# Optimization experiments

Measured on AMD Instinct MI355X. Metric: run time of the kernel, lower is better.

## Reference

```python
import jax, jax.numpy as jnp
import numpy as np

B, S, D, F, E, NS, K = 2, 1024, 1024, 4096, 8, 8, 2
FS = F // NS  # shared-expert hidden size = d_ff // num_shared_experts


def setup_inputs() -> dict:
    key = jax.random.key(0)
    ks = jax.random.split(key, 8)
    scale = 0.02
    return {
        "hidden_states": jax.random.normal(ks[0], (B, S, D), jnp.float32),
        "gate_W": jax.random.normal(ks[1], (E, D), jnp.float32) * scale,
        "w1_e": jax.random.normal(ks[2], (E, D, F), jnp.float32) * scale,
        "w3_e": jax.random.normal(ks[3], (E, D, F), jnp.float32) * scale,
        "w2_e": jax.random.normal(ks[4], (E, F, D), jnp.float32) * scale,
        "w1_s": jax.random.normal(ks[5], (NS, D, FS), jnp.float32) * scale,
        "w3_s": jax.random.normal(ks[6], (NS, D, FS), jnp.float32) * scale,
        "w2_s": jax.random.normal(ks[7], (NS, FS, D), jnp.float32) * scale,
    }


def reference(hidden_states, gate_W, w1_e, w3_e, w2_e, w1_s, w3_s, w2_s):
    b, s, d = hidden_states.shape
    e = gate_W.shape[0]
    flat = hidden_states.reshape(-1, d)            # [T, D]
    T = flat.shape[0]

    # --- gate: softmax over experts, top-k probs scattered (k=0 slot only survives) ---
    logits = (flat @ gate_W.T).astype(jnp.float32)  # [T, E]
    probs = jax.nn.softmax(logits, axis=-1)
    top_v, top_i = jax.lax.top_k(probs, K)          # [T, K]
    gates = jnp.zeros((T, e), probs.dtype).at[jnp.arange(T)[:, None], top_i].set(top_v)

    # --- routed experts: module runs every expert densely on all tokens ---
    g = jax.nn.silu(jnp.einsum('td,edf->etf', flat, w1_e))  # [E, T, F]
    u = jnp.einsum('td,edf->etf', flat, w3_e)
    out_e = jnp.einsum('etf,efd->etd', g * u, w2_e)         # [E, T, D]
    routed = jnp.einsum('te,etd->td', gates, out_e).reshape(b, s, d)

    # --- shared experts (mean over NS experts) ---
    gs = jax.nn.silu(jnp.einsum('bsd,ndf->nbsf', hidden_states, w1_s))
    us = jnp.einsum('bsd,ndf->nbsf', hidden_states, w3_s)
    shared = jnp.einsum('nbsf,nfd->bsd', gs * us, w2_s) / w1_s.shape[0]

    alpha = 0.5
    return alpha * shared + (1.0 - alpha) * routed
```

## Files before the change

kernel.cpp:

```cpp
#include <hip/hip_runtime.h>

#define T 2048
#define D 1024
#define F 4096
#define E 8
#define NS 8
#define FS 512
#define SHB 5120
#define NROWS 7168
#define MT_MAX 56

typedef float floatx4 __attribute__((ext_vector_type(4)));
typedef short short8 __attribute__((ext_vector_type(8)));

__device__ __forceinline__ unsigned short f2bf(float f) {
  unsigned int u = __float_as_uint(f);
  u += 0x7FFF + ((u >> 16) & 1);
  return (unsigned short)(u >> 16);
}

__device__ __forceinline__ void glds16(const void* g, void* l) {
  __builtin_amdgcn_global_load_lds(
      (const __attribute__((address_space(1))) void*)g,
      (__attribute__((address_space(3))) void*)l, 16, 0, 0);
}

__global__ void gate_kernel(const float* __restrict__ x, const float* __restrict__ gW,
                            unsigned short* __restrict__ xb, int* __restrict__ cnt,
                            int* __restrict__ list_tok, float* __restrict__ list_gate) {
  int t = blockIdx.x, tid = threadIdx.x;
  const float* xr = x + (size_t)t * D;
  float acc[E];
#pragma unroll
  for (int e = 0; e < E; ++e) acc[e] = 0.f;
  for (int d = tid; d < D; d += 256) {
    float xv = xr[d];
    xb[(size_t)t * D + d] = f2bf(xv);
#pragma unroll
    for (int e = 0; e < E; ++e) acc[e] += xv * gW[e * D + d];
  }
#pragma unroll
  for (int o = 32; o > 0; o >>= 1)
#pragma unroll
    for (int e = 0; e < E; ++e) acc[e] += __shfl_down(acc[e], o, 64);
  __shared__ float wred[4][E];
  int lane = tid & 63, wv = tid >> 6;
  if (lane == 0)
#pragma unroll
    for (int e = 0; e < E; ++e) wred[wv][e] = acc[e];
  __syncthreads();
  if (tid == 0) {
    float l[E];
#pragma unroll
    for (int e = 0; e < E; ++e) l[e] = wred[0][e] + wred[1][e] + wred[2][e] + wred[3][e];
    int i1 = 0; float m1 = l[0];
    for (int e = 1; e < E; ++e) if (l[e] > m1) { m1 = l[e]; i1 = e; }
    int i2 = -1; float m2 = -3.4e38f;
    for (int e = 0; e < E; ++e) if (e != i1 && l[e] > m2) { m2 = l[e]; i2 = e; }
    float s = 0.f, p[E];
#pragma unroll
    for (int e = 0; e < E; ++e) { p[e] = __expf(l[e] - m1); s += p[e]; }
    float inv = 1.f / s;
    int p1 = atomicAdd(&cnt[i1], 1);
    list_tok[i1 * T + p1] = t; list_gate[i1 * T + p1] = p[i1] * inv;
    int p2 = atomicAdd(&cnt[i2], 1);
    list_tok[i2 * T + p2] = t; list_gate[i2 * T + p2] = p[i2] * inv;
  }
}

__global__ void offsets_kernel(const int* __restrict__ cnt, int* __restrict__ off,
                               int* __restrict__ mt_expert) {
  if (threadIdx.x == 0 && blockIdx.x == 0) {
    int o = 0;
    for (int e = 0; e < E; ++e) { off[e] = o; o += (cnt[e] + 127) & ~127; }
    off[E] = o;
    for (int i = 0; i < MT_MAX; ++i) mt_expert[i] = -1;
    for (int e = 0; e < E; ++e) {
      int t0 = off[e] >> 7, nt = (cnt[e] + 127) >> 7;
      for (int i = 0; i < nt; ++i) mt_expert[t0 + i] = e;
    }
    for (int i = SHB >> 7; i < MT_MAX; ++i) mt_expert[i] = E;
  }
}

__global__ void scatter_kernel(const int* __restrict__ cnt, const int* __restrict__ off,
                               const int* __restrict__ list_tok, const float* __restrict__ list_gate,
                               int* __restrict__ tok_of_row, float* __restrict__ row_scale,
                               int* __restrict__ tok_rows, int* __restrict__ tk) {
  int idx = blockIdx.x * 256 + threadIdx.x;
  int e = idx >> 11, i = idx & (T - 1);
  if (e < E && i < cnt[e]) {
    int row = off[e] + i;
    int t = list_tok[e * T + i];
    tok_of_row[row] = t;
    row_scale[row] = 0.5f * list_gate[e * T + i];
    int k = atomicAdd(&tk[t], 1);
    tok_rows[2 * t + k] = row;
  }
}

__global__ void transpose_cast(const float* __restrict__ in, unsigned short* __restrict__ out,
                               int R, int C) {
  in += (size_t)blockIdx.z * R * C;
  out += (size_t)blockIdx.z * R * C;
  int r0 = blockIdx.y * 32, c0 = blockIdx.x * 32;
  __shared__ float tile[32][33];
  int tid = threadIdx.x;
#pragma unroll
  for (int p = 0; p < 4; ++p) {
    int idx = p * 256 + tid;
    int rl = idx >> 5, cl = idx & 31;
    tile[rl][cl] = in[(size_t)(r0 + rl) * C + c0 + cl];
  }
  __syncthreads();
  int Rt = R >> 5;
#pragma unroll
  for (int p = 0; p < 4; ++p) {
    int idx = p * 256 + tid;
    int cl = idx >> 5, rl = idx & 31;
    int c = c0 + cl, r = r0 + rl;
    size_t o = ((size_t)(c >> 7) * Rt + (r >> 5)) * 4096 + (size_t)(c & 127) * 32 + (r & 31);
    out[o] = f2bf(tile[rl][cl]);
  }
}

__global__ __launch_bounds__(256, 2) void up_gemm(
    const unsigned short* __restrict__ xb, const unsigned short* __restrict__ W1T,
    const unsigned short* __restrict__ W3T, const unsigned short* __restrict__ W1sT,
    const unsigned short* __restrict__ W3sT, const int* __restrict__ cnt,
    const int* __restrict__ off, const int* __restrict__ tok_of_row,
    unsigned short* __restrict__ Hb) {
  int e = blockIdx.z, mtile = blockIdx.y, ntile = blockIdx.x;
  int hbase;
  const unsigned short *B1, *B3;
  if (e < E) {
    int Me = cnt[e];
    if (mtile * 128 >= Me) return;
    hbase = off[e];
    B1 = W1T + (size_t)e * F * D;
    B3 = W3T + (size_t)e * F * D;
  } else {
    hbase = SHB;
    B1 = W1sT; B3 = W3sT;
  }
  __shared__ unsigned short Al[128 * 32];
  __shared__ unsigned short B1l[128 * 32];
  __shared__ unsigned short B3l[128 * 32];
  int tid = threadIdx.x;
  int lane = tid & 63, wv = tid >> 6, wm = wv >> 1, wn = wv & 1;
  int row16 = lane & 15, quad = lane >> 4;

  int ar = tid >> 1;
  int lrow = mtile * 128 + ar;
  int srow = (e < E) ? tok_of_row[hbase + lrow] : lrow;
  const uint4* aptr = (const uint4*)(xb + (size_t)srow * D) + (tid & 1) * 2;
  uint4* alds = (uint4*)Al + ar * 4 + (tid & 1) * 2;

  const unsigned short* b1t = B1 + (size_t)ntile * (D / 32) * 4096;
  const unsigned short* b3t = B3 + (size_t)ntile * (D / 32) * 4096;

  floatx4 accg[4][4], accu[4][4];
#pragma unroll
  for (int i = 0; i < 4; ++i)
#pragma unroll
    for (int j = 0; j < 4; ++j) {
      accg[i][j] = (floatx4){0.f, 0.f, 0.f, 0.f};
      accu[i][j] = (floatx4){0.f, 0.f, 0.f, 0.f};
    }
  int lw = wv * 1024;
  for (int kt = 0; kt < D / 32; ++kt) {
    uint4 av0 = aptr[0];
    uint4 av1 = aptr[1];
    const char* b1s = (const char*)(b1t + (size_t)kt * 4096);
    const char* b3s = (const char*)(b3t + (size_t)kt * 4096);
    glds16(b1s + tid * 16, (char*)B1l + lw);
    glds16(b1s + 4096 + tid * 16, (char*)B1l + 4096 + lw);
    glds16(b3s + tid * 16, (char*)B3l + lw);
    glds16(b3s + 4096 + tid * 16, (char*)B3l + 4096 + lw);
    alds[0] = av0; alds[1] = av1;
    __syncthreads();
    short8 af[4], b1f[4], b3f[4];
#pragma unroll
    for (int mi = 0; mi < 4; ++mi)
      af[mi] = *(const short8*)(Al + (wm * 64 + mi * 16 + row16) * 32 + quad * 8);
#pragma unroll
    for (int ni = 0; ni < 4; ++ni) {
      b1f[ni] = *(const short8*)(B1l + (wn * 64 + ni * 16 + row16) * 32 + quad * 8);
      b3f[ni] = *(const short8*)(B3l + (wn * 64 + ni * 16 + row16) * 32 + quad * 8);
    }
#pragma unroll
    for (int mi = 0; mi < 4; ++mi)
#pragma unroll
      for (int ni = 0; ni < 4; ++ni) {
        accg[mi][ni] = __builtin_amdgcn_mfma_f32_16x16x32_bf16(af[mi], b1f[ni], accg[mi][ni], 0, 0, 0);
        accu[mi][ni] = __builtin_amdgcn_mfma_f32_16x16x32_bf16(af[mi], b3f[ni], accu[mi][ni], 0, 0, 0);
      }
    aptr += 4;
    __syncthreads();
  }
#pragma unroll
  for (int mi = 0; mi < 4; ++mi)
#pragma unroll
    for (int ni = 0; ni < 4; ++ni)
#pragma unroll
      for (int r = 0; r < 4; ++r) {
        int lr = mtile * 128 + wm * 64 + mi * 16 + quad * 4 + r;
        int hrow = hbase + lr;
        int col = ntile * 128 + wn * 64 + ni * 16 + row16;
        float g = accg[mi][ni][r], u = accu[mi][ni][r];
        float h = g * u / (1.0f + __expf(-g));
        size_t o = ((size_t)(hrow >> 7) * 128 + (col >> 5)) * 4096 + (size_t)(hrow & 127) * 32 + (col & 31);
        Hb[o] = f2bf(h);
      }
}

__global__ __launch_bounds__(256, 2) void down_gemm(
    const unsigned short* __restrict__ Hb, const unsigned short* __restrict__ W2T,
    const unsigned short* __restrict__ W2sT, const int* __restrict__ mt_expert,
    const float* __restrict__ row_scale, float* __restrict__ O) {
  int mt = blockIdx.y, ntile = blockIdx.x;
  int e = mt_expert[mt];
  if (e < 0) return;
  const unsigned short* Bt = ((e < E) ? (W2T + (size_t)e * D * F) : W2sT)
                             + (size_t)ntile * (F / 32) * 4096;
  const unsigned short* At = Hb + (size_t)mt * (F / 32) * 4096;
  __shared__ unsigned short Al[128 * 32];
  __shared__ unsigned short Bl[128 * 32];
  int tid = threadIdx.x;
  int lane = tid & 63, wv = tid >> 6, wm = wv >> 1, wn = wv & 1;
  int row16 = lane & 15, quad = lane >> 4;
  floatx4 acc[4][4];
#pragma unroll
  for (int i = 0; i < 4; ++i)
#pragma unroll
    for (int j = 0; j < 4; ++j) acc[i][j] = (floatx4){0.f, 0.f, 0.f, 0.f};
  int lw = wv * 1024;
  for (int kt = 0; kt < F / 32; ++kt) {
    const char* as = (const char*)(At + (size_t)kt * 4096);
    const char* bs = (const char*)(Bt + (size_t)kt * 4096);
    glds16(as + tid * 16, (char*)Al + lw);
    glds16(as + 4096 + tid * 16, (char*)Al + 4096 + lw);
    glds16(bs + tid * 16, (char*)Bl + lw);
    glds16(bs + 4096 + tid * 16, (char*)Bl + 4096 + lw);
    __syncthreads();
    short8 af[4], bf[4];
#pragma unroll
    for (int mi = 0; mi < 4; ++mi)
      af[mi] = *(const short8*)(Al + (wm * 64 + mi * 16 + row16) * 32 + quad * 8);
#pragma unroll
    for (int ni = 0; ni < 4; ++ni)
      bf[ni] = *(const short8*)(Bl + (wn * 64 + ni * 16 + row16) * 32 + quad * 8);
#pragma unroll
    for (int mi = 0; mi < 4; ++mi)
#pragma unroll
      for (int ni = 0; ni < 4; ++ni)
        acc[mi][ni] = __builtin_amdgcn_mfma_f32_16x16x32_bf16(af[mi], bf[ni], acc[mi][ni], 0, 0, 0);
    __syncthreads();
  }
#pragma unroll
  for (int mi = 0; mi < 4; ++mi)
#pragma unroll
    for (int ni = 0; ni < 4; ++ni)
#pragma unroll
      for (int r = 0; r < 4; ++r) {
        int grow = mt * 128 + wm * 64 + mi * 16 + quad * 4 + r;
        int col = ntile * 128 + wn * 64 + ni * 16 + row16;
        float scale = (grow < SHB) ? row_scale[grow] : 0.0625f;
        O[(size_t)grow * D + col] = acc[mi][ni][r] * scale;
      }
}

__global__ void combine_kernel(const float* __restrict__ O, const int* __restrict__ tok_rows,
                               float* __restrict__ out) {
  int idx = blockIdx.x * 256 + threadIdx.x;
  int t = idx >> 8, c = idx & 255;
  int r0 = tok_rows[2 * t], r1 = tok_rows[2 * t + 1];
  const float4* O4 = (const float4*)O;
  float4 a = O4[(size_t)r0 * 256 + c];
  float4 b = O4[(size_t)r1 * 256 + c];
  float4 s = O4[((size_t)SHB + t) * 256 + c];
  float4 r;
  r.x = a.x + b.x + s.x;
  r.y = a.y + b.y + s.y;
  r.z = a.z + b.z + s.z;
  r.w = a.w + b.w + s.w;
  ((float4*)out)[idx] = r;
}

extern "C" void kernel_launch(void* const* d_in, const int* in_sizes, int n_in,
                              void* d_out, int out_size, void* d_ws, size_t ws_size,
                              hipStream_t stream) {
  (void)in_sizes; (void)n_in; (void)out_size; (void)ws_size;
  const float* x   = (const float*)d_in[0];
  const float* gW  = (const float*)d_in[1];
  const float* w1e = (const float*)d_in[2];
  const float* w3e = (const float*)d_in[3];
  const float* w2e = (const float*)d_in[4];
  const float* w1s = (const float*)d_in[5];
  const float* w3s = (const float*)d_in[6];
  const float* w2s = (const float*)d_in[7];
  float* out = (float*)d_out;

  char* w = (char*)d_ws;
  auto alloc = [&](size_t bytes) {
    char* p = w; w += (bytes + 255) & ~(size_t)255; return p;
  };
  unsigned short* xb   = (unsigned short*)alloc((size_t)T * D * 2);
  unsigned short* W1T  = (unsigned short*)alloc((size_t)E * F * D * 2);
  unsigned short* W3T  = (unsigned short*)alloc((size_t)E * F * D * 2);
  unsigned short* W2T  = (unsigned short*)alloc((size_t)E * D * F * 2);
  unsigned short* W1sT = (unsigned short*)alloc((size_t)F * D * 2);
  unsigned short* W3sT = (unsigned short*)alloc((size_t)F * D * 2);
  unsigned short* W2sT = (unsigned short*)alloc((size_t)D * F * 2);
  unsigned short* Hb   = (unsigned short*)alloc((size_t)NROWS * F * 2);
  float* Ob        = (float*)alloc((size_t)NROWS * D * 4);
  float* row_scale = (float*)alloc((size_t)SHB * 4);
  float* list_gate = (float*)alloc((size_t)E * T * 4);
  int* list_tok    = (int*)alloc((size_t)E * T * 4);
  int* tok_rows    = (int*)alloc((size_t)T * 2 * 4);
  int* offv        = (int*)alloc(16 * 4);
  int* mt_expert   = (int*)alloc(64 * 4);
  int* ctrl        = (int*)alloc((size_t)(8 + T + SHB) * 4);
  int* cnt = ctrl; int* tk = ctrl + 8; int* tok_of_row = ctrl + 8 + T;

  hipMemsetAsync(ctrl, 0, (size_t)(8 + T + SHB) * 4, stream);
  gate_kernel<<<T, 256, 0, stream>>>(x, gW, xb, cnt, list_tok, list_gate);
  offsets_kernel<<<1, 64, 0, stream>>>(cnt, offv, mt_expert);
  scatter_kernel<<<(E * T) / 256, 256, 0, stream>>>(cnt, offv, list_tok, list_gate,
                                                    tok_of_row, row_scale, tok_rows, tk);
  transpose_cast<<<dim3(F / 32, D / 32, E), 256, 0, stream>>>(w1e, W1T, D, F);
  transpose_cast<<<dim3(F / 32, D / 32, E), 256, 0, stream>>>(w3e, W3T, D, F);
  transpose_cast<<<dim3(D / 32, F / 32, E), 256, 0, stream>>>(w2e, W2T, F, D);
  transpose_cast<<<dim3(FS / 32, D / 32, NS), 256, 0, stream>>>(w1s, W1sT, D, FS);
  transpose_cast<<<dim3(FS / 32, D / 32, NS), 256, 0, stream>>>(w3s, W3sT, D, FS);
  transpose_cast<<<dim3(D / 32, F / 32, 1), 256, 0, stream>>>(w2s, W2sT, F, D);
  up_gemm<<<dim3(F / 128, 16, E + 1), 256, 0, stream>>>(xb, W1T, W3T, W1sT, W3sT,
                                                        cnt, offv, tok_of_row, Hb);
  down_gemm<<<dim3(D / 128, MT_MAX), 256, 0, stream>>>(Hb, W2T, W2sT, mt_expert, row_scale, Ob);
  combine_kernel<<<(T * D / 4) / 256, 256, 0, stream>>>(Ob, tok_rows, out);
}
```

Baseline: 777.3 us.

## Swizzle LDS tiles, split-K down GEMM, compact up grid, vectorize transpose

The transpose-cast kernel now uses float4 loads and ushort4 stores. Both GEMMs XOR-swizzle their LDS layout to avoid bank conflicts on the fragment reads. The up GEMM launches only live m-tiles through the mt_expert map. The down GEMM is split along K into two halves that write separate output buffers, which the combine kernel sums. Split-K doubles the down GEMM's parallelism but costs an extra fp32 output buffer plus more traffic in combine.

Measured after the change: 745.2 us. 1.04x faster.

```diff
diff --git a/kernel.cpp b/kernel.cpp
--- a/kernel.cpp
+++ b/kernel.cpp
@@ -106,41 +106,38 @@
   int r0 = blockIdx.y * 32, c0 = blockIdx.x * 32;
   __shared__ float tile[32][33];
   int tid = threadIdx.x;
-#pragma unroll
-  for (int p = 0; p < 4; ++p) {
-    int idx = p * 256 + tid;
-    int rl = idx >> 5, cl = idx & 31;
-    tile[rl][cl] = in[(size_t)(r0 + rl) * C + c0 + cl];
+  {
+    int rl = tid >> 3, cl = (tid & 7) * 4;
+    float4 v = *(const float4*)(in + (size_t)(r0 + rl) * C + c0 + cl);
+    tile[rl][cl] = v.x; tile[rl][cl + 1] = v.y;
+    tile[rl][cl + 2] = v.z; tile[rl][cl + 3] = v.w;
   }
   __syncthreads();
-  int Rt = R >> 5;
-#pragma unroll
-  for (int p = 0; p < 4; ++p) {
-    int idx = p * 256 + tid;
-    int cl = idx >> 5, rl = idx & 31;
-    int c = c0 + cl, r = r0 + rl;
+  {
+    int cl = tid >> 3, rq = (tid & 7) * 4;
+    int c = c0 + cl, r = r0 + rq;
+    ushort4 v;
+    v.x = f2bf(tile[rq][cl]);     v.y = f2bf(tile[rq + 1][cl]);
+    v.z = f2bf(tile[rq + 2][cl]); v.w = f2bf(tile[rq + 3][cl]);
+    int Rt = R >> 5;
     size_t o = ((size_t)(c >> 7) * Rt + (r >> 5)) * 4096 + (size_t)(c & 127) * 32 + (r & 31);
-    out[o] = f2bf(tile[rl][cl]);
+    *(ushort4*)(out + o) = v;
   }
 }
 
 __global__ __launch_bounds__(256, 2) void up_gemm(
     const unsigned short* __restrict__ xb, const unsigned short* __restrict__ W1T,
     const unsigned short* __restrict__ W3T, const unsigned short* __restrict__ W1sT,
-    const unsigned short* __restrict__ W3sT, const int* __restrict__ cnt,
-    const int* __restrict__ off, const int* __restrict__ tok_of_row,
-    unsigned short* __restrict__ Hb) {
-  int e = blockIdx.z, mtile = blockIdx.y, ntile = blockIdx.x;
-  int hbase;
+    const unsigned short* __restrict__ W3sT, const int* __restrict__ mt_expert,
+    const int* __restrict__ tok_of_row, unsigned short* __restrict__ Hb) {
+  int mt = blockIdx.y, ntile = blockIdx.x;
+  int e = mt_expert[mt];
+  if (e < 0) return;
   const unsigned short *B1, *B3;
   if (e < E) {
-    int Me = cnt[e];
-    if (mtile * 128 >= Me) return;
-    hbase = off[e];
     B1 = W1T + (size_t)e * F * D;
     B3 = W3T + (size_t)e * F * D;
   } else {
-    hbase = SHB;
     B1 = W1sT; B3 = W3sT;
   }
   __shared__ unsigned short Al[128 * 32];
@@ -149,12 +146,17 @@
   int tid = threadIdx.x;
   int lane = tid & 63, wv = tid >> 6, wm = wv >> 1, wn = wv & 1;
   int row16 = lane & 15, quad = lane >> 4;
+  int qsw8 = ((lane >> 4) ^ ((lane >> 1) & 3)) * 8;
+  int swzb = (tid & ~3) * 16 + (((tid & 3) ^ ((tid >> 3) & 3)) * 16);
 
   int ar = tid >> 1;
-  int lrow = mtile * 128 + ar;
-  int srow = (e < E) ? tok_of_row[hbase + lrow] : lrow;
-  const uint4* aptr = (const uint4*)(xb + (size_t)srow * D) + (tid & 1) * 2;
-  uint4* alds = (uint4*)Al + ar * 4 + (tid & 1) * 2;
+  int hrow_s = mt * 128 + ar;
+  int srow = (e < E) ? tok_of_row[hrow_s] : (hrow_s - SHB);
+  int ja = (tid & 1) * 2;
+  int sa = (tid >> 2) & 3;
+  const uint4* aptr = (const uint4*)(xb + (size_t)srow * D) + ja;
+  uint4* alds0 = (uint4*)Al + ar * 4 + (ja ^ sa);
+  uint4* alds1 = (uint4*)Al + ar * 4 + ((ja + 1) ^ sa);
 
   const unsigned short* b1t = B1 + (size_t)ntile * (D / 32) * 4096;
   const unsigned short* b3t = B3 + (size_t)ntile * (D / 32) * 4096;
@@ -173,20 +175,20 @@
     uint4 av1 = aptr[1];
     const char* b1s = (const char*)(b1t + (size_t)kt * 4096);
     const char* b3s = (const char*)(b3t + (size_t)kt * 4096);
-    glds16(b1s + tid * 16, (char*)B1l + lw);
-    glds16(b1s + 4096 + tid * 16, (char*)B1l + 4096 + lw);
-    glds16(b3s + tid * 16, (char*)B3l + lw);
-    glds16(b3s + 4096 + tid * 16, (char*)B3l + 4096 + lw);
-    alds[0] = av0; alds[1] = av1;
+    glds16(b1s + swzb, (char*)B1l + lw);
+    glds16(b1s + 4096 + swzb, (char*)B1l + 4096 + lw);
+    glds16(b3s + swzb, (char*)B3l + lw);
+    glds16(b3s + 4096 + swzb, (char*)B3l + 4096 + lw);
+    alds0[0] = av0; alds1[0] = av1;
     __syncthreads();
     short8 af[4], b1f[4], b3f[4];
 #pragma unroll
     for (int mi = 0; mi < 4; ++mi)
-      af[mi] = *(const short8*)(Al + (wm * 64 + mi * 16 + row16) * 32 + quad * 8);
+      af[mi] = *(const short8*)(Al + (wm * 64 + mi * 16 + row16) * 32 + qsw8);
 #pragma unroll
     for (int ni = 0; ni < 4; ++ni) {
-      b1f[ni] = *(const short8*)(B1l + (wn * 64 + ni * 16 + row16) * 32 + quad * 8);
-      b3f[ni] = *(const short8*)(B3l + (wn * 64 + ni * 16 + row16) * 32 + quad * 8);
+      b1f[ni] = *(const short8*)(B1l + (wn * 64 + ni * 16 + row16) * 32 + qsw8);
+      b3f[ni] = *(const short8*)(B3l + (wn * 64 + ni * 16 + row16) * 32 + qsw8);
     }
 #pragma unroll
     for (int mi = 0; mi < 4; ++mi)
@@ -204,8 +206,7 @@
     for (int ni = 0; ni < 4; ++ni)
 #pragma unroll
       for (int r = 0; r < 4; ++r) {
-        int lr = mtile * 128 + wm * 64 + mi * 16 + quad * 4 + r;
-        int hrow = hbase + lr;
+        int hrow = mt * 128 + wm * 64 + mi * 16 + quad * 4 + r;
         int col = ntile * 128 + wn * 64 + ni * 16 + row16;
         float g = accg[mi][ni][r], u = accu[mi][ni][r];
         float h = g * u / (1.0f + __expf(-g));
@@ -218,38 +219,41 @@
     const unsigned short* __restrict__ Hb, const unsigned short* __restrict__ W2T,
     const unsigned short* __restrict__ W2sT, const int* __restrict__ mt_expert,
     const float* __restrict__ row_scale, float* __restrict__ O) {
-  int mt = blockIdx.y, ntile = blockIdx.x;
+  int mt = blockIdx.y, ntile = blockIdx.x, kz = blockIdx.z;
   int e = mt_expert[mt];
   if (e < 0) return;
   const unsigned short* Bt = ((e < E) ? (W2T + (size_t)e * D * F) : W2sT)
                              + (size_t)ntile * (F / 32) * 4096;
   const unsigned short* At = Hb + (size_t)mt * (F / 32) * 4096;
+  O += (size_t)kz * NROWS * D;
   __shared__ unsigned short Al[128 * 32];
   __shared__ unsigned short Bl[128 * 32];
   int tid = threadIdx.x;
   int lane = tid & 63, wv = tid >> 6, wm = wv >> 1, wn = wv & 1;
   int row16 = lane & 15, quad = lane >> 4;
+  int qsw8 = ((lane >> 4) ^ ((lane >> 1) & 3)) * 8;
+  int swzb = (tid & ~3) * 16 + (((tid & 3) ^ ((tid >> 3) & 3)) * 16);
   floatx4 acc[4][4];
 #pragma unroll
   for (int i = 0; i < 4; ++i)
 #pragma unroll
     for (int j = 0; j < 4; ++j) acc[i][j] = (floatx4){0.f, 0.f, 0.f, 0.f};
   int lw = wv * 1024;
-  for (int kt = 0; kt < F / 32; ++kt) {
+  for (int kt = kz * 64; kt < kz * 64 + 64; ++kt) {
     const char* as = (const char*)(At + (size_t)kt * 4096);
     const char* bs = (const char*)(Bt + (size_t)kt * 4096);
-    glds16(as + tid * 16, (char*)Al + lw);
-    glds16(as + 4096 + tid * 16, (char*)Al + 4096 + lw);
-    glds16(bs + tid * 16, (char*)Bl + lw);
-    glds16(bs + 4096 + tid * 16, (char*)Bl + 4096 + lw);
+    glds16(as + swzb, (char*)Al + lw);
+    glds16(as + 4096 + swzb, (char*)Al + 4096 + lw);
+    glds16(bs + swzb, (char*)Bl + lw);
+    glds16(bs + 4096 + swzb, (char*)Bl + 4096 + lw);
     __syncthreads();
     short8 af[4], bf[4];
 #pragma unroll
     for (int mi = 0; mi < 4; ++mi)
-      af[mi] = *(const short8*)(Al + (wm * 64 + mi * 16 + row16) * 32 + quad * 8);
+      af[mi] = *(const short8*)(Al + (wm * 64 + mi * 16 + row16) * 32 + qsw8);
 #pragma unroll
     for (int ni = 0; ni < 4; ++ni)
-      bf[ni] = *(const short8*)(Bl + (wn * 64 + ni * 16 + row16) * 32 + quad * 8);
+      bf[ni] = *(const short8*)(Bl + (wn * 64 + ni * 16 + row16) * 32 + qsw8);
 #pragma unroll
     for (int mi = 0; mi < 4; ++mi)
 #pragma unroll
@@ -276,14 +280,18 @@
   int t = idx >> 8, c = idx & 255;
   int r0 = tok_rows[2 * t], r1 = tok_rows[2 * t + 1];
   const float4* O4 = (const float4*)O;
+  const size_t HLF = (size_t)NROWS * 256;
   float4 a = O4[(size_t)r0 * 256 + c];
   float4 b = O4[(size_t)r1 * 256 + c];
   float4 s = O4[((size_t)SHB + t) * 256 + c];
+  float4 a2 = O4[HLF + (size_t)r0 * 256 + c];
+  float4 b2 = O4[HLF + (size_t)r1 * 256 + c];
+  float4 s2 = O4[HLF + ((size_t)SHB + t) * 256 + c];
   float4 r;
-  r.x = a.x + b.x + s.x;
-  r.y = a.y + b.y + s.y;
-  r.z = a.z + b.z + s.z;
-  r.w = a.w + b.w + s.w;
+  r.x = a.x + b.x + s.x + a2.x + b2.x + s2.x;
+  r.y = a.y + b.y + s.y + a2.y + b2.y + s2.y;
+  r.z = a.z + b.z + s.z + a2.z + b2.z + s2.z;
+  r.w = a.w + b.w + s.w + a2.w + b2.w + s2.w;
   ((float4*)out)[idx] = r;
 }
 
@@ -313,7 +321,7 @@
   unsigned short* W3sT = (unsigned short*)alloc((size_t)F * D * 2);
   unsigned short* W2sT = (unsigned short*)alloc((size_t)D * F * 2);
   unsigned short* Hb   = (unsigned short*)alloc((size_t)NROWS * F * 2);
-  float* Ob        = (float*)alloc((size_t)NROWS * D * 4);
+  float* Ob        = (float*)alloc((size_t)2 * NROWS * D * 4);
   float* row_scale = (float*)alloc((size_t)SHB * 4);
   float* list_gate = (float*)alloc((size_t)E * T * 4);
   int* list_tok    = (int*)alloc((size_t)E * T * 4);
@@ -334,8 +342,8 @@
   transpose_cast<<<dim3(FS / 32, D / 32, NS), 256, 0, stream>>>(w1s, W1sT, D, FS);
   transpose_cast<<<dim3(FS / 32, D / 32, NS), 256, 0, stream>>>(w3s, W3sT, D, FS);
   transpose_cast<<<dim3(D / 32, F / 32, 1), 256, 0, stream>>>(w2s, W2sT, F, D);
-  up_gemm<<<dim3(F / 128, 16, E + 1), 256, 0, stream>>>(xb, W1T, W3T, W1sT, W3sT,
-                                                        cnt, offv, tok_of_row, Hb);
-  down_gemm<<<dim3(D / 128, MT_MAX), 256, 0, stream>>>(Hb, W2T, W2sT, mt_expert, row_scale, Ob);
+  up_gemm<<<dim3(F / 128, MT_MAX), 256, 0, stream>>>(xb, W1T, W3T, W1sT, W3sT,
+                                                     mt_expert, tok_of_row, Hb);
+  down_gemm<<<dim3(D / 128, MT_MAX, 2), 256, 0, stream>>>(Hb, W2T, W2sT, mt_expert, row_scale, Ob);
   combine_kernel<<<(T * D / 4) / 256, 256, 0, stream>>>(Ob, tok_rows, out);
 }
```
